# Performance work log

Measured on AMD Instinct MI355X. Metric: run time of the kernel, lower is better.

The kernel has to match this reference:

```python
import jax, jax.numpy as jnp
import numpy as np

EPS = 1e-5
NUM_GROUPS = 8


def group_norm(x, gamma, beta):
    # x: [B, C, T]; normalize per group over (C/G, T)
    B, C, T = x.shape
    G = NUM_GROUPS
    xg = x.reshape(B, G, C // G, T)
    mean = xg.mean(axis=(2, 3), keepdims=True)
    var = xg.var(axis=(2, 3), keepdims=True)
    xn = ((xg - mean) * jax.lax.rsqrt(var + EPS)).reshape(B, C, T)
    return xn * gamma[None, :, None] + beta[None, :, None]


def mish(x):
    return x * jnp.tanh(jax.nn.softplus(x))


def setup_inputs() -> dict:
    key = jax.random.key(0)
    ks = jax.random.split(key, 7)
    C, Cb, B, T = 1024, 256, 64, 512
    # conv1d kernel_size=1 weights stored as [out, in]
    w_down = jax.random.normal(ks[0], (Cb, C), dtype=jnp.float32) / np.sqrt(C)
    b_down = jax.random.normal(ks[1], (Cb,), dtype=jnp.float32) * 0.01
    w_up = jax.random.normal(ks[2], (C, Cb), dtype=jnp.float32) / np.sqrt(Cb)
    b_up = jax.random.normal(ks[3], (C,), dtype=jnp.float32) * 0.01
    gamma = jnp.ones((C,), dtype=jnp.float32)
    beta = jnp.zeros((C,), dtype=jnp.float32)
    x = jax.random.normal(ks[4], (B, C, T), dtype=jnp.float32)
    return {"x": x, "gamma": gamma, "beta": beta,
            "w_down": w_down, "b_down": b_down,
            "w_up": w_up, "b_up": b_up}


def reference(x, gamma, beta, w_down, b_down, w_up, b_up):
    residual = x
    h = group_norm(x, gamma, beta)                       # [B, C, T]
    h = jnp.einsum('bct,oc->bot', h, w_down) + b_down[None, :, None]  # [B, Cb, T]
    h = mish(h)
    h = jnp.einsum('bct,oc->bot', h, w_up) + b_up[None, :, None]      # [B, C, T]
    return h + residual
```

## Files before the change

### kernel.cpp

```cpp
#include <hip/hip_runtime.h>
#include <hip/hip_bf16.h>
#include <stddef.h>

#define B_   64
#define C_   1024
#define CB_  256
#define T_   512
#define G_   8
#define N_   32768
#define EPS_ 1e-5f

using short8 = __attribute__((ext_vector_type(8))) short;
using f32x4  = __attribute__((ext_vector_type(4))) float;

__device__ __forceinline__ short f2bf(float f) {
    unsigned u = __float_as_uint(f);
    u += 0x7fffu + ((u >> 16) & 1u);
    return (short)(u >> 16);
}

__device__ __forceinline__ float mish_f(float y) {
    float u = __expf(fminf(y, 30.f));
    float w = u * u + 2.f * u;
    return y * (w / (w + 2.f));
}

__global__ void prep_weights(const float* __restrict__ wd, const float* __restrict__ wu,
                             short* __restrict__ wdb, short* __restrict__ wub) {
    int i = blockIdx.x * 256 + threadIdx.x;
    if (i < CB_ * C_) {
        wdb[i] = f2bf(wd[i]);
        wub[i] = f2bf(wu[i]);
    }
}

__global__ void stats_kernel(const float* __restrict__ x, const float* __restrict__ gamma,
                             const float* __restrict__ beta,
                             float* __restrict__ scaleW, float* __restrict__ shiftW) {
    const int tid = threadIdx.x;
    const int bg = blockIdx.x;
    const int b = bg >> 3, g = bg & 7;
    const float4* p = (const float4*)(x + ((size_t)b * C_ + g * 128) * T_);
    float s = 0.f, q = 0.f;
    for (int i = tid; i < 16384; i += 256) {
        float4 v = p[i];
        s += v.x + v.y + v.z + v.w;
        q += v.x * v.x + v.y * v.y + v.z * v.z + v.w * v.w;
    }
    for (int o = 32; o > 0; o >>= 1) {
        s += __shfl_down(s, o);
        q += __shfl_down(q, o);
    }
    __shared__ float red[8];
    __shared__ float mr[2];
    const int wid = tid >> 6, lane = tid & 63;
    if (lane == 0) { red[wid] = s; red[4 + wid] = q; }
    __syncthreads();
    if (tid == 0) {
        float S = red[0] + red[1] + red[2] + red[3];
        float Q = red[4] + red[5] + red[6] + red[7];
        float mean = S * (1.f / 65536.f);
        float var = Q * (1.f / 65536.f) - mean * mean;
        mr[0] = mean;
        mr[1] = rsqrtf(var + EPS_);
    }
    __syncthreads();
    float mean = mr[0], rstd = mr[1];
    if (tid < 128) {
        int c = g * 128 + tid;
        float sc = rstd * gamma[c];
        scaleW[b * C_ + c] = sc;
        shiftW[b * C_ + c] = beta[c] - mean * sc;
    }
}

#define LDSTR 40

__global__ __launch_bounds__(256, 2) void gemm1_mish(
    const float* __restrict__ x, const short* __restrict__ wd,
    const float* __restrict__ b_down,
    const float* __restrict__ scaleW, const float* __restrict__ shiftW,
    short* __restrict__ mid) {
    __shared__ short As[128 * LDSTR];
    __shared__ short Bs[128 * LDSTR];
    __shared__ float sS[C_], sT[C_];

    const int tid = threadIdx.x;
    const int n0 = blockIdx.x * 128;
    const int m0 = blockIdx.y * 128;
    const int b  = n0 >> 9;

    for (int i = tid; i < C_; i += 256) {
        sS[i] = scaleW[b * C_ + i];
        sT[i] = shiftW[b * C_ + i];
    }

    const int a_kc = tid & 3;
    const int a_m  = tid >> 2;
    const int b_n  = tid & 127;
    const int b_kg = tid >> 7;
    const int wid  = tid >> 6;
    const int lane = tid & 63;
    const int wm = wid >> 1, wn = wid & 1;
    const int q = lane >> 4, l16 = lane & 15;

    f32x4 acc[4][4];
#pragma unroll
    for (int i = 0; i < 4; i++)
#pragma unroll
        for (int j = 0; j < 4; j++) acc[i][j] = 0.f;

    const float* xb = x + (size_t)b * C_ * T_ + (n0 & 511);

    for (int kt = 0; kt < 32; ++kt) {
        const int k0 = kt * 32;
        __syncthreads();
        {
            const short* src = wd + (m0 + a_m) * C_ + k0 + a_kc * 8;
            *(short8*)&As[a_m * LDSTR + a_kc * 8] = *(const short8*)src;
            *(short8*)&As[(a_m + 64) * LDSTR + a_kc * 8] = *(const short8*)(src + 64 * C_);
        }
        {
            const int cbase = k0 + b_kg * 16;
            const float* xp = xb + (size_t)cbase * T_ + b_n;
            f32x4 ss[4], st[4];
#pragma unroll
            for (int i2 = 0; i2 < 4; i2++) {
                ss[i2] = *(const f32x4*)&sS[cbase + i2 * 4];
                st[i2] = *(const f32x4*)&sT[cbase + i2 * 4];
            }
            short8 v0, v1;
#pragma unroll
            for (int i = 0; i < 8; i++) {
                float h0 = xp[(size_t)i * T_] * ss[i >> 2][i & 3] + st[i >> 2][i & 3];
                v0[i] = f2bf(h0);
            }
#pragma unroll
            for (int i = 0; i < 8; i++) {
                int k = i + 8;
                float h1 = xp[(size_t)k * T_] * ss[k >> 2][k & 3] + st[k >> 2][k & 3];
                v1[i] = f2bf(h1);
            }
            *(short8*)&Bs[b_n * LDSTR + b_kg * 16] = v0;
            *(short8*)&Bs[b_n * LDSTR + b_kg * 16 + 8] = v1;
        }
        __syncthreads();
        short8 af[4], bfr[4];
#pragma unroll
        for (int i = 0; i < 4; i++)
            af[i] = *(const short8*)&As[(wm * 64 + i * 16 + l16) * LDSTR + q * 8];
#pragma unroll
        for (int j = 0; j < 4; j++)
            bfr[j] = *(const short8*)&Bs[(wn * 64 + j * 16 + l16) * LDSTR + q * 8];
#pragma unroll
        for (int i = 0; i < 4; i++)
#pragma unroll
            for (int j = 0; j < 4; j++)
                acc[i][j] = __builtin_amdgcn_mfma_f32_16x16x32_bf16(af[i], bfr[j], acc[i][j], 0, 0, 0);
    }
#pragma unroll
    for (int i = 0; i < 4; i++) {
        const int o_b = m0 + wm * 64 + i * 16 + q * 4;
#pragma unroll
        for (int j = 0; j < 4; j++) {
            const int n = n0 + wn * 64 + j * 16 + l16;
#pragma unroll
            for (int r = 0; r < 4; r++) {
                const int o = o_b + r;
                float y = acc[i][j][r] + b_down[o];
                mid[(size_t)o * N_ + n] = f2bf(mish_f(y));
            }
        }
    }
}

__global__ __launch_bounds__(256, 2) void gemm2_resid(
    const short* __restrict__ mid, const short* __restrict__ wu,
    const float* __restrict__ b_up, const float* __restrict__ x,
    float* __restrict__ out) {
    __shared__ short As[128 * LDSTR];
    __shared__ short Bs[128 * LDSTR];

    const int tid = threadIdx.x;
    const int n0 = blockIdx.x * 128;
    const int m0 = blockIdx.y * 128;

    const int a_kc = tid & 3;
    const int a_m  = tid >> 2;
    const int b_n  = tid & 127;
    const int b_kg = tid >> 7;
    const int wid  = tid >> 6;
    const int lane = tid & 63;
    const int wm = wid >> 1, wn = wid & 1;
    const int q = lane >> 4, l16 = lane & 15;

    f32x4 acc[4][4];
#pragma unroll
    for (int i = 0; i < 4; i++)
#pragma unroll
        for (int j = 0; j < 4; j++) acc[i][j] = 0.f;

    for (int kt = 0; kt < 8; ++kt) {
        const int k0 = kt * 32;
        __syncthreads();
        {
            const short* src = wu + (m0 + a_m) * CB_ + k0 + a_kc * 8;
            *(short8*)&As[a_m * LDSTR + a_kc * 8] = *(const short8*)src;
            *(short8*)&As[(a_m + 64) * LDSTR + a_kc * 8] = *(const short8*)(src + 64 * CB_);
        }
        {
            const short* mp = mid + (size_t)(k0 + b_kg * 16) * N_ + n0 + b_n;
            short8 v0, v1;
#pragma unroll
            for (int i = 0; i < 8; i++) v0[i] = mp[(size_t)i * N_];
#pragma unroll
            for (int i = 0; i < 8; i++) v1[i] = mp[(size_t)(i + 8) * N_];
            *(short8*)&Bs[b_n * LDSTR + b_kg * 16] = v0;
            *(short8*)&Bs[b_n * LDSTR + b_kg * 16 + 8] = v1;
        }
        __syncthreads();
        short8 af[4], bfr[4];
#pragma unroll
        for (int i = 0; i < 4; i++)
            af[i] = *(const short8*)&As[(wm * 64 + i * 16 + l16) * LDSTR + q * 8];
#pragma unroll
        for (int j = 0; j < 4; j++)
            bfr[j] = *(const short8*)&Bs[(wn * 64 + j * 16 + l16) * LDSTR + q * 8];
#pragma unroll
        for (int i = 0; i < 4; i++)
#pragma unroll
            for (int j = 0; j < 4; j++)
                acc[i][j] = __builtin_amdgcn_mfma_f32_16x16x32_bf16(af[i], bfr[j], acc[i][j], 0, 0, 0);
    }
    const int b = n0 >> 9;
    const int t0 = n0 & 511;
#pragma unroll
    for (int i = 0; i < 4; i++) {
        const int c_b = m0 + wm * 64 + i * 16 + q * 4;
#pragma unroll
        for (int j = 0; j < 4; j++) {
            const int tt = t0 + wn * 64 + j * 16 + l16;
#pragma unroll
            for (int r = 0; r < 4; r++) {
                const int c = c_b + r;
                const size_t gi = ((size_t)b * C_ + c) * T_ + tt;
                out[gi] = acc[i][j][r] + b_up[c] + x[gi];
            }
        }
    }
}

extern "C" void kernel_launch(void* const* d_in, const int* in_sizes, int n_in,
                              void* d_out, int out_size, void* d_ws, size_t ws_size,
                              hipStream_t stream) {
    const float* x      = (const float*)d_in[0];
    const float* gamma  = (const float*)d_in[1];
    const float* beta   = (const float*)d_in[2];
    const float* w_down = (const float*)d_in[3];
    const float* b_down = (const float*)d_in[4];
    const float* w_up   = (const float*)d_in[5];
    const float* b_up   = (const float*)d_in[6];
    float* out = (float*)d_out;

    float* scaleW = (float*)d_ws;
    float* shiftW = scaleW + B_ * C_;
    short* wdb    = (short*)(shiftW + B_ * C_);
    short* wub    = wdb + CB_ * C_;
    short* mid    = wub + C_ * CB_;

    prep_weights<<<dim3((CB_ * C_ + 255) / 256), 256, 0, stream>>>(w_down, w_up, wdb, wub);
    stats_kernel<<<dim3(B_ * G_), 256, 0, stream>>>(x, gamma, beta, scaleW, shiftW);
    gemm1_mish<<<dim3(N_ / 128, CB_ / 128), 256, 0, stream>>>(x, wdb, b_down, scaleW, shiftW, mid);
    gemm2_resid<<<dim3(N_ / 128, C_ / 128), 256, 0, stream>>>(mid, wub, b_up, x, out);
}
```

Baseline: 339.8 us.

## Prefetch next K-tile in registers and widen gemm1 tile to full Cb

Both GEMM kernels now load the next K-slice of weights and activations into registers while MFMAs run on the current shared-memory tile, then write it to LDS after a barrier. gemm1 uses 512 threads covering all 256 output channels per block, so x is read and normalised once instead of twice. gemm2 swaps grid axes so consecutive blocks share the same mid columns, and loads mid with paired 32-bit reads. This adds register pressure and a larger block that may reduce occupancy.

```diff
diff --git a/kernel.cpp b/kernel.cpp
--- a/kernel.cpp
+++ b/kernel.cpp
@@ -76,21 +76,20 @@
 
 #define LDSTR 40
 
-__global__ __launch_bounds__(256, 2) void gemm1_mish(
+__global__ __launch_bounds__(512, 2) void gemm1_mish(
     const float* __restrict__ x, const short* __restrict__ wd,
     const float* __restrict__ b_down,
     const float* __restrict__ scaleW, const float* __restrict__ shiftW,
     short* __restrict__ mid) {
-    __shared__ short As[128 * LDSTR];
+    __shared__ short As[256 * LDSTR];
     __shared__ short Bs[128 * LDSTR];
     __shared__ float sS[C_], sT[C_];
 
     const int tid = threadIdx.x;
     const int n0 = blockIdx.x * 128;
-    const int m0 = blockIdx.y * 128;
     const int b  = n0 >> 9;
 
-    for (int i = tid; i < C_; i += 256) {
+    for (int i = tid; i < C_; i += 512) {
         sS[i] = scaleW[b * C_ + i];
         sT[i] = shiftW[b * C_ + i];
     }
@@ -112,39 +111,38 @@
 
     const float* xb = x + (size_t)b * C_ * T_ + (n0 & 511);
 
+    short8 a0, a1;
+    float bv[8];
+    {
+        const short* src = wd + a_m * C_ + a_kc * 8;
+        a0 = *(const short8*)src;
+        a1 = *(const short8*)(src + 128 * C_);
+        const float* xp = xb + (size_t)(b_kg * 8) * T_ + b_n;
+#pragma unroll
+        for (int i = 0; i < 8; i++) bv[i] = xp[(size_t)i * T_];
+    }
+    __syncthreads();
+    {
+        *(short8*)&As[a_m * LDSTR + a_kc * 8] = a0;
+        *(short8*)&As[(a_m + 128) * LDSTR + a_kc * 8] = a1;
+        short8 v;
+        const int kb = b_kg * 8;
+#pragma unroll
+        for (int i = 0; i < 8; i++) v[i] = f2bf(bv[i] * sS[kb + i] + sT[kb + i]);
+        *(short8*)&Bs[b_n * LDSTR + kb] = v;
+    }
+    __syncthreads();
+
     for (int kt = 0; kt < 32; ++kt) {
-        const int k0 = kt * 32;
-        __syncthreads();
-        {
-            const short* src = wd + (m0 + a_m) * C_ + k0 + a_kc * 8;
-            *(short8*)&As[a_m * LDSTR + a_kc * 8] = *(const short8*)src;
-            *(short8*)&As[(a_m + 64) * LDSTR + a_kc * 8] = *(const short8*)(src + 64 * C_);
-        }
-        {
-            const int cbase = k0 + b_kg * 16;
-            const float* xp = xb + (size_t)cbase * T_ + b_n;
-            f32x4 ss[4], st[4];
-#pragma unroll
-            for (int i2 = 0; i2 < 4; i2++) {
-                ss[i2] = *(const f32x4*)&sS[cbase + i2 * 4];
-                st[i2] = *(const f32x4*)&sT[cbase + i2 * 4];
-            }
-            short8 v0, v1;
-#pragma unroll
-            for (int i = 0; i < 8; i++) {
-                float h0 = xp[(size_t)i * T_] * ss[i >> 2][i & 3] + st[i >> 2][i & 3];
-                v0[i] = f2bf(h0);
-            }
-#pragma unroll
-            for (int i = 0; i < 8; i++) {
-                int k = i + 8;
-                float h1 = xp[(size_t)k * T_] * ss[k >> 2][k & 3] + st[k >> 2][k & 3];
-                v1[i] = f2bf(h1);
-            }
-            *(short8*)&Bs[b_n * LDSTR + b_kg * 16] = v0;
-            *(short8*)&Bs[b_n * LDSTR + b_kg * 16 + 8] = v1;
-        }
-        __syncthreads();
+        if (kt < 31) {
+            const int k1 = (kt + 1) * 32;
+            const short* src = wd + a_m * C_ + k1 + a_kc * 8;
+            a0 = *(const short8*)src;
+            a1 = *(const short8*)(src + 128 * C_);
+            const float* xp = xb + (size_t)(k1 + b_kg * 8) * T_ + b_n;
+#pragma unroll
+            for (int i = 0; i < 8; i++) bv[i] = xp[(size_t)i * T_];
+        }
         short8 af[4], bfr[4];
 #pragma unroll
         for (int i = 0; i < 4; i++)
@@ -157,10 +155,23 @@
 #pragma unroll
             for (int j = 0; j < 4; j++)
                 acc[i][j] = __builtin_amdgcn_mfma_f32_16x16x32_bf16(af[i], bfr[j], acc[i][j], 0, 0, 0);
-    }
+        __syncthreads();
+        if (kt < 31) {
+            *(short8*)&As[a_m * LDSTR + a_kc * 8] = a0;
+            *(short8*)&As[(a_m + 128) * LDSTR + a_kc * 8] = a1;
+            short8 v;
+            const int kb = (kt + 1) * 32 + b_kg * 8;
+            const int kl = b_kg * 8;
+#pragma unroll
+            for (int i = 0; i < 8; i++) v[i] = f2bf(bv[i] * sS[kb + i] + sT[kb + i]);
+            *(short8*)&Bs[b_n * LDSTR + kl] = v;
+        }
+        __syncthreads();
+    }
+
 #pragma unroll
     for (int i = 0; i < 4; i++) {
-        const int o_b = m0 + wm * 64 + i * 16 + q * 4;
+        const int o_b = wm * 64 + i * 16 + q * 4;
 #pragma unroll
         for (int j = 0; j < 4; j++) {
             const int n = n0 + wn * 64 + j * 16 + l16;
@@ -182,13 +193,13 @@
     __shared__ short Bs[128 * LDSTR];
 
     const int tid = threadIdx.x;
-    const int n0 = blockIdx.x * 128;
-    const int m0 = blockIdx.y * 128;
+    const int m0 = blockIdx.x * 128;
+    const int n0 = blockIdx.y * 128;
 
     const int a_kc = tid & 3;
     const int a_m  = tid >> 2;
-    const int b_n  = tid & 127;
-    const int b_kg = tid >> 7;
+    const int b_np = tid & 63;
+    const int b_kg = tid >> 6;
     const int wid  = tid >> 6;
     const int lane = tid & 63;
     const int wm = wid >> 1, wn = wid & 1;
@@ -200,25 +211,37 @@
 #pragma unroll
         for (int j = 0; j < 4; j++) acc[i][j] = 0.f;
 
+    short8 a0, a1;
+    ushort2 bv[8];
+    {
+        const short* src = wu + (m0 + a_m) * CB_ + a_kc * 8;
+        a0 = *(const short8*)src;
+        a1 = *(const short8*)(src + 64 * CB_);
+        const unsigned short* mp = (const unsigned short*)mid + (size_t)(b_kg * 8) * N_ + n0 + b_np * 2;
+#pragma unroll
+        for (int i = 0; i < 8; i++) bv[i] = *(const ushort2*)(mp + (size_t)i * N_);
+    }
+    {
+        *(short8*)&As[a_m * LDSTR + a_kc * 8] = a0;
+        *(short8*)&As[(a_m + 64) * LDSTR + a_kc * 8] = a1;
+        short8 v0, v1;
+#pragma unroll
+        for (int i = 0; i < 8; i++) { v0[i] = (short)bv[i].x; v1[i] = (short)bv[i].y; }
+        *(short8*)&Bs[(b_np * 2) * LDSTR + b_kg * 8] = v0;
+        *(short8*)&Bs[(b_np * 2 + 1) * LDSTR + b_kg * 8] = v1;
+    }
+    __syncthreads();
+
     for (int kt = 0; kt < 8; ++kt) {
-        const int k0 = kt * 32;
-        __syncthreads();
-        {
-            const short* src = wu + (m0 + a_m) * CB_ + k0 + a_kc * 8;
-            *(short8*)&As[a_m * LDSTR + a_kc * 8] = *(const short8*)src;
-            *(short8*)&As[(a_m + 64) * LDSTR + a_kc * 8] = *(const short8*)(src + 64 * CB_);
-        }
-        {
-            const short* mp = mid + (size_t)(k0 + b_kg * 16) * N_ + n0 + b_n;
-            short8 v0, v1;
-#pragma unroll
-            for (int i = 0; i < 8; i++) v0[i] = mp[(size_t)i * N_];
-#pragma unroll
-            for (int i = 0; i < 8; i++) v1[i] = mp[(size_t)(i + 8) * N_];
-            *(short8*)&Bs[b_n * LDSTR + b_kg * 16] = v0;
-            *(short8*)&Bs[b_n * LDSTR + b_kg * 16 + 8] = v1;
-        }
-        __syncthreads();
+        if (kt < 7) {
+            const int k1 = (kt + 1) * 32;
+            const short* src = wu + (m0 + a_m) * CB_ + k1 + a_kc * 8;
+            a0 = *(const short8*)src;
+            a1 = *(const short8*)(src + 64 * CB_);
+            const unsigned short* mp = (const unsigned short*)mid + (size_t)(k1 + b_kg * 8) * N_ + n0 + b_np * 2;
+#pragma unroll
+            for (int i = 0; i < 8; i++) bv[i] = *(const ushort2*)(mp + (size_t)i * N_);
+        }
         short8 af[4], bfr[4];
 #pragma unroll
         for (int i = 0; i < 4; i++)
@@ -231,7 +254,19 @@
 #pragma unroll
             for (int j = 0; j < 4; j++)
                 acc[i][j] = __builtin_amdgcn_mfma_f32_16x16x32_bf16(af[i], bfr[j], acc[i][j], 0, 0, 0);
-    }
+        __syncthreads();
+        if (kt < 7) {
+            *(short8*)&As[a_m * LDSTR + a_kc * 8] = a0;
+            *(short8*)&As[(a_m + 64) * LDSTR + a_kc * 8] = a1;
+            short8 v0, v1;
+#pragma unroll
+            for (int i = 0; i < 8; i++) { v0[i] = (short)bv[i].x; v1[i] = (short)bv[i].y; }
+            *(short8*)&Bs[(b_np * 2) * LDSTR + b_kg * 8] = v0;
+            *(short8*)&Bs[(b_np * 2 + 1) * LDSTR + b_kg * 8] = v1;
+        }
+        __syncthreads();
+    }
+
     const int b = n0 >> 9;
     const int t0 = n0 & 511;
 #pragma unroll
@@ -270,6 +305,6 @@
 
     prep_weights<<<dim3((CB_ * C_ + 255) / 256), 256, 0, stream>>>(w_down, w_up, wdb, wub);
     stats_kernel<<<dim3(B_ * G_), 256, 0, stream>>>(x, gamma, beta, scaleW, shiftW);
-    gemm1_mish<<<dim3(N_ / 128, CB_ / 128), 256, 0, stream>>>(x, wdb, b_down, scaleW, shiftW, mid);
-    gemm2_resid<<<dim3(N_ / 128, C_ / 128), 256, 0, stream>>>(mid, wub, b_up, x, out);
-}
+    gemm1_mish<<<dim3(N_ / 128), 512, 0, stream>>>(x, wdb, b_down, scaleW, shiftW, mid);
+    gemm2_resid<<<dim3(C_ / 128, N_ / 128), 256, 0, stream>>>(mid, wub, b_up, x, out);
+}
```

Measured after the change: 331.2 us. -2.5%, faster.

## Double-buffer GEMM tiles with direct global-to-LDS loads and transpose mid layout

Applied to the files above, without the earlier changes.

Both GEMMs now double-buffer their shared-memory tiles and use global_load_lds to copy weight tiles straight into LDS while the current tile is multiplied. The intermediate activation is stored as [N, Cb] instead of [Cb, N], so gemm2 can load it with contiguous 16-byte direct loads rather than strided 2-byte gathers. The grid order is swapped so neighbouring blocks share the same N columns, which should improve L2 reuse of x and mid. gemm2 also raises its launch bound for more occupancy. The extra barriers and the larger LDS footprint may cost some latency or occupancy in exchange.

```diff
diff --git a/kernel.cpp b/kernel.cpp
--- a/kernel.cpp
+++ b/kernel.cpp
@@ -10,8 +10,9 @@
 #define N_   32768
 #define EPS_ 1e-5f
 
-using short8 = __attribute__((ext_vector_type(8))) short;
-using f32x4  = __attribute__((ext_vector_type(4))) float;
+using short8  = __attribute__((ext_vector_type(8))) short;
+using short4v = __attribute__((ext_vector_type(4))) short;
+using f32x4   = __attribute__((ext_vector_type(4))) float;
 
 __device__ __forceinline__ short f2bf(float f) {
     unsigned u = __float_as_uint(f);
@@ -23,6 +24,12 @@
     float u = __expf(fminf(y, 30.f));
     float w = u * u + 2.f * u;
     return y * (w / (w + 2.f));
+}
+
+__device__ __forceinline__ void load_lds16(const void* g, void* l) {
+    __builtin_amdgcn_global_load_lds(
+        (__attribute__((address_space(1))) void*)g,
+        (__attribute__((address_space(3))) void*)l, 16, 0, 0);
 }
 
 __global__ void prep_weights(const float* __restrict__ wd, const float* __restrict__ wu,
@@ -42,6 +49,7 @@
     const int b = bg >> 3, g = bg & 7;
     const float4* p = (const float4*)(x + ((size_t)b * C_ + g * 128) * T_);
     float s = 0.f, q = 0.f;
+#pragma unroll 4
     for (int i = tid; i < 16384; i += 256) {
         float4 v = p[i];
         s += v.x + v.y + v.z + v.w;
@@ -81,13 +89,13 @@
     const float* __restrict__ b_down,
     const float* __restrict__ scaleW, const float* __restrict__ shiftW,
     short* __restrict__ mid) {
-    __shared__ short As[128 * LDSTR];
+    __shared__ short Abuf[2][4096];
     __shared__ short Bs[128 * LDSTR];
     __shared__ float sS[C_], sT[C_];
 
-    const int tid = threadIdx.x;
-    const int n0 = blockIdx.x * 128;
-    const int m0 = blockIdx.y * 128;
+    const int tid = threadIdx.x, lane = tid & 63, wid = tid >> 6;
+    const int m0 = blockIdx.x * 128;
+    const int n0 = blockIdx.y * 128;
     const int b  = n0 >> 9;
 
     for (int i = tid; i < C_; i += 256) {
@@ -95,12 +103,8 @@
         sT[i] = shiftW[b * C_ + i];
     }
 
-    const int a_kc = tid & 3;
-    const int a_m  = tid >> 2;
     const int b_n  = tid & 127;
-    const int b_kg = tid >> 7;
-    const int wid  = tid >> 6;
-    const int lane = tid & 63;
+    const int b_kh = tid >> 7;
     const int wm = wid >> 1, wn = wid & 1;
     const int q = lane >> 4, l16 = lane & 15;
 
@@ -110,45 +114,54 @@
 #pragma unroll
         for (int j = 0; j < 4; j++) acc[i][j] = 0.f;
 
-    const float* xb = x + (size_t)b * C_ * T_ + (n0 & 511);
+    const float* xb  = x + (size_t)b * C_ * T_ + (n0 & 511);
+    const short* wdm = wd + (size_t)m0 * C_;
+
+    float bv[16];
+
+#define ISSUE_A(k0, bufi)                                                       \
+    {                                                                           \
+        _Pragma("unroll")                                                       \
+        for (int u = 0; u < 2; u++) {                                           \
+            int iid = wid * 2 + u, c = iid >> 1, h = iid & 1;                   \
+            load_lds16(wdm + (size_t)(h * 64 + lane) * C_ + (k0) + c * 8,       \
+                       &Abuf[bufi][(c * 128 + h * 64) * 8]);                    \
+        }                                                                       \
+    }
+#define LOAD_B(k0)                                                              \
+    {                                                                           \
+        const float* xp = xb + (size_t)((k0) + b_kh * 16) * T_ + b_n;           \
+        _Pragma("unroll")                                                       \
+        for (int i = 0; i < 16; i++) bv[i] = xp[(size_t)i * T_];                \
+    }
+#define WRITE_B(k0)                                                             \
+    {                                                                           \
+        const int kb = (k0) + b_kh * 16;                                        \
+        short8 v0, v1;                                                          \
+        _Pragma("unroll")                                                       \
+        for (int i = 0; i < 8; i++) v0[i] = f2bf(bv[i] * sS[kb + i] + sT[kb + i]); \
+        _Pragma("unroll")                                                       \
+        for (int i = 0; i < 8; i++) v1[i] = f2bf(bv[8 + i] * sS[kb + 8 + i] + sT[kb + 8 + i]); \
+        *(short8*)&Bs[b_n * LDSTR + b_kh * 16] = v0;                            \
+        *(short8*)&Bs[b_n * LDSTR + b_kh * 16 + 8] = v1;                        \
+    }
+
+    ISSUE_A(0, 0);
+    LOAD_B(0);
+    __syncthreads();
+    WRITE_B(0);
+    __syncthreads();
 
     for (int kt = 0; kt < 32; ++kt) {
-        const int k0 = kt * 32;
-        __syncthreads();
-        {
-            const short* src = wd + (m0 + a_m) * C_ + k0 + a_kc * 8;
-            *(short8*)&As[a_m * LDSTR + a_kc * 8] = *(const short8*)src;
-            *(short8*)&As[(a_m + 64) * LDSTR + a_kc * 8] = *(const short8*)(src + 64 * C_);
+        if (kt < 31) {
+            ISSUE_A((kt + 1) * 32, (kt + 1) & 1);
+            LOAD_B((kt + 1) * 32);
         }
-        {
-            const int cbase = k0 + b_kg * 16;
-            const float* xp = xb + (size_t)cbase * T_ + b_n;
-            f32x4 ss[4], st[4];
-#pragma unroll
-            for (int i2 = 0; i2 < 4; i2++) {
-                ss[i2] = *(const f32x4*)&sS[cbase + i2 * 4];
-                st[i2] = *(const f32x4*)&sT[cbase + i2 * 4];
-            }
-            short8 v0, v1;
-#pragma unroll
-            for (int i = 0; i < 8; i++) {
-                float h0 = xp[(size_t)i * T_] * ss[i >> 2][i & 3] + st[i >> 2][i & 3];
-                v0[i] = f2bf(h0);
-            }
-#pragma unroll
-            for (int i = 0; i < 8; i++) {
-                int k = i + 8;
-                float h1 = xp[(size_t)k * T_] * ss[k >> 2][k & 3] + st[k >> 2][k & 3];
-                v1[i] = f2bf(h1);
-            }
-            *(short8*)&Bs[b_n * LDSTR + b_kg * 16] = v0;
-            *(short8*)&Bs[b_n * LDSTR + b_kg * 16 + 8] = v1;
-        }
-        __syncthreads();
+        const short* Ab = Abuf[kt & 1];
         short8 af[4], bfr[4];
 #pragma unroll
         for (int i = 0; i < 4; i++)
-            af[i] = *(const short8*)&As[(wm * 64 + i * 16 + l16) * LDSTR + q * 8];
+            af[i] = *(const short8*)&Ab[(q * 128 + wm * 64 + i * 16 + l16) * 8];
 #pragma unroll
         for (int j = 0; j < 4; j++)
             bfr[j] = *(const short8*)&Bs[(wn * 64 + j * 16 + l16) * LDSTR + q * 8];
@@ -157,40 +170,41 @@
 #pragma unroll
             for (int j = 0; j < 4; j++)
                 acc[i][j] = __builtin_amdgcn_mfma_f32_16x16x32_bf16(af[i], bfr[j], acc[i][j], 0, 0, 0);
-    }
+        __syncthreads();
+        if (kt < 31) WRITE_B((kt + 1) * 32);
+        __syncthreads();
+    }
+
 #pragma unroll
     for (int i = 0; i < 4; i++) {
-        const int o_b = m0 + wm * 64 + i * 16 + q * 4;
+        const int o0 = m0 + wm * 64 + i * 16 + q * 4;
+        float bd0 = b_down[o0], bd1 = b_down[o0 + 1], bd2 = b_down[o0 + 2], bd3 = b_down[o0 + 3];
 #pragma unroll
         for (int j = 0; j < 4; j++) {
             const int n = n0 + wn * 64 + j * 16 + l16;
-#pragma unroll
-            for (int r = 0; r < 4; r++) {
-                const int o = o_b + r;
-                float y = acc[i][j][r] + b_down[o];
-                mid[(size_t)o * N_ + n] = f2bf(mish_f(y));
-            }
+            short4v v;
+            v[0] = f2bf(mish_f(acc[i][j][0] + bd0));
+            v[1] = f2bf(mish_f(acc[i][j][1] + bd1));
+            v[2] = f2bf(mish_f(acc[i][j][2] + bd2));
+            v[3] = f2bf(mish_f(acc[i][j][3] + bd3));
+            *(short4v*)&mid[(size_t)n * CB_ + o0] = v;
         }
     }
-}
-
-__global__ __launch_bounds__(256, 2) void gemm2_resid(
+#undef ISSUE_A
+#undef LOAD_B
+#undef WRITE_B
+}
+
+__global__ __launch_bounds__(256, 4) void gemm2_resid(
     const short* __restrict__ mid, const short* __restrict__ wu,
     const float* __restrict__ b_up, const float* __restrict__ x,
     float* __restrict__ out) {
-    __shared__ short As[128 * LDSTR];
-    __shared__ short Bs[128 * LDSTR];
-
-    const int tid = threadIdx.x;
-    const int n0 = blockIdx.x * 128;
-    const int m0 = blockIdx.y * 128;
-
-    const int a_kc = tid & 3;
-    const int a_m  = tid >> 2;
-    const int b_n  = tid & 127;
-    const int b_kg = tid >> 7;
-    const int wid  = tid >> 6;
-    const int lane = tid & 63;
+    __shared__ short Abuf[2][4096];
+    __shared__ short Bbuf[2][4096];
+
+    const int tid = threadIdx.x, lane = tid & 63, wid = tid >> 6;
+    const int m0 = blockIdx.x * 128;
+    const int n0 = blockIdx.y * 128;
     const int wm = wid >> 1, wn = wid & 1;
     const int q = lane >> 4, l16 = lane & 15;
 
@@ -200,38 +214,49 @@
 #pragma unroll
         for (int j = 0; j < 4; j++) acc[i][j] = 0.f;
 
+    const short* wum = wu + (size_t)m0 * CB_;
+    const short* mb  = mid + (size_t)n0 * CB_;
+
+#define ISSUE_AB(k0, bufi)                                                        \
+    {                                                                             \
+        _Pragma("unroll")                                                         \
+        for (int u = 0; u < 4; u++) {                                             \
+            int iid = wid * 4 + u;                                                \
+            if (iid < 8) {                                                        \
+                int c = iid >> 1, h = iid & 1;                                    \
+                load_lds16(wum + (size_t)(h * 64 + lane) * CB_ + (k0) + c * 8,    \
+                           &Abuf[bufi][(c * 128 + h * 64) * 8]);                  \
+            } else {                                                              \
+                int jj = iid - 8, c = jj >> 1, h = jj & 1;                        \
+                load_lds16(mb + (size_t)(h * 64 + lane) * CB_ + (k0) + c * 8,     \
+                           &Bbuf[bufi][(c * 128 + h * 64) * 8]);                  \
+            }                                                                     \
+        }                                                                         \
+    }
+
+    ISSUE_AB(0, 0);
+    __syncthreads();
+
     for (int kt = 0; kt < 8; ++kt) {
-        const int k0 = kt * 32;
-        __syncthreads();
-        {
-            const short* src = wu + (m0 + a_m) * CB_ + k0 + a_kc * 8;
-            *(short8*)&As[a_m * LDSTR + a_kc * 8] = *(const short8*)src;
-            *(short8*)&As[(a_m + 64) * LDSTR + a_kc * 8] = *(const short8*)(src + 64 * CB_);
-        }
-        {
-            const short* mp = mid + (size_t)(k0 + b_kg * 16) * N_ + n0 + b_n;
-            short8 v0, v1;
-#pragma unroll
-            for (int i = 0; i < 8; i++) v0[i] = mp[(size_t)i * N_];
-#pragma unroll
-            for (int i = 0; i < 8; i++) v1[i] = mp[(size_t)(i + 8) * N_];
-            *(short8*)&Bs[b_n * LDSTR + b_kg * 16] = v0;
-            *(short8*)&Bs[b_n * LDSTR + b_kg * 16 + 8] = v1;
-        }
-        __syncthreads();
+        if (kt < 7) ISSUE_AB((kt + 1) * 32, (kt + 1) & 1);
+        const short* Ab = Abuf[kt & 1];
+        const short* Bb = Bbuf[kt & 1];
         short8 af[4], bfr[4];
 #pragma unroll
         for (int i = 0; i < 4; i++)
-            af[i] = *(const short8*)&As[(wm * 64 + i * 16 + l16) * LDSTR + q * 8];
+            af[i] = *(const short8*)&Ab[(q * 128 + wm * 64 + i * 16 + l16) * 8];
 #pragma unroll
         for (int j = 0; j < 4; j++)
-            bfr[j] = *(const short8*)&Bs[(wn * 64 + j * 16 + l16) * LDSTR + q * 8];
+            bfr[j] = *(const short8*)&Bb[(q * 128 + wn * 64 + j * 16 + l16) * 8];
 #pragma unroll
         for (int i = 0; i < 4; i++)
 #pragma unroll
             for (int j = 0; j < 4; j++)
                 acc[i][j] = __builtin_amdgcn_mfma_f32_16x16x32_bf16(af[i], bfr[j], acc[i][j], 0, 0, 0);
-    }
+        __syncthreads();
+    }
+#undef ISSUE_AB
+
     const int b = n0 >> 9;
     const int t0 = n0 & 511;
 #pragma unroll
@@ -270,6 +295,6 @@
 
     prep_weights<<<dim3((CB_ * C_ + 255) / 256), 256, 0, stream>>>(w_down, w_up, wdb, wub);
     stats_kernel<<<dim3(B_ * G_), 256, 0, stream>>>(x, gamma, beta, scaleW, shiftW);
-    gemm1_mish<<<dim3(N_ / 128, CB_ / 128), 256, 0, stream>>>(x, wdb, b_down, scaleW, shiftW, mid);
-    gemm2_resid<<<dim3(N_ / 128, C_ / 128), 256, 0, stream>>>(mid, wub, b_up, x, out);
-}
+    gemm1_mish<<<dim3(2, N_ / 128), 256, 0, stream>>>(x, wdb, b_down, scaleW, shiftW, mid);
+    gemm2_resid<<<dim3(C_ / 128, N_ / 128), 256, 0, stream>>>(mid, wub, b_up, x, out);
+}
```

Measured after the change: 387.5 us. 14.1% more time.
